# Kernel optimization log

Hardware: AMD Instinct MI355X
Metric: run time of the kernel (lower is better)

Reference implementation:

```python
import jax, jax.numpy as jnp
import numpy as np

N_HEAD = 16

def setup_inputs() -> dict:
    key = jax.random.key(0)
    ks = jax.random.split(key, 9)
    B, T, C = 4, 2048, 1024
    s = 1.0 / np.sqrt(C)
    return {
        "x":  jax.random.normal(ks[0], (B, T, C), jnp.float32),
        "Wq": jax.random.normal(ks[1], (C, C), jnp.float32) * s,
        "bq": jax.random.normal(ks[2], (C,), jnp.float32) * 0.02,
        "Wk": jax.random.normal(ks[3], (C, C), jnp.float32) * s,
        "bk": jax.random.normal(ks[4], (C,), jnp.float32) * 0.02,
        "Wv": jax.random.normal(ks[5], (C, C), jnp.float32) * s,
        "bv": jax.random.normal(ks[6], (C,), jnp.float32) * 0.02,
        "Wp": jax.random.normal(ks[7], (C, C), jnp.float32) * s,
        "bp": jax.random.normal(ks[8], (C,), jnp.float32) * 0.02,
    }

def reference(x, Wq, bq, Wk, bk, Wv, bv, Wp, bp):
    B, T, C = x.shape
    H, D = N_HEAD, C // N_HEAD
    # torch nn.Linear: y = x @ W^T + b
    q = (x @ Wq.T + bq).reshape(B, T, H, D).transpose(0, 2, 1, 3)  # [B,H,T,D]
    k = (x @ Wk.T + bk).reshape(B, T, H, D).transpose(0, 2, 1, 3)
    v = (x @ Wv.T + bv).reshape(B, T, H, D).transpose(0, 2, 1, 3)
    # full TxT causal attention (non-flash path)
    att = jnp.einsum('bhtd,bhsd->bhts', q, k) * (1.0 / np.sqrt(D))  # [B,H,T,T]
    causal = jnp.tril(jnp.ones((T, T), dtype=bool))
    att = jnp.where(causal[None, None], att, -jnp.inf)
    att = jax.nn.softmax(att, axis=-1)
    y = jnp.einsum('bhts,bhsd->bhtd', att, v)  # [B,H,T,D]
    y = y.transpose(0, 2, 1, 3).reshape(B, T, C)
    return y @ Wp.T + bp
```

## Files before the change

kernel.cpp:

```cpp
#include <hip/hip_runtime.h>

typedef __bf16 bf16_t;
typedef __bf16 bf16x8 __attribute__((ext_vector_type(8)));
typedef float f32x4 __attribute__((ext_vector_type(4)));
typedef unsigned short ushort_t;

#define T_SEQ 2048
#define C_DIM 1024
#define NH    16
#define HD    64

__device__ __forceinline__ ushort_t f2bf(float f) {
    unsigned u = __builtin_bit_cast(unsigned, f);
    u += 0x7FFFu + ((u >> 16) & 1u);
    return (ushort_t)(u >> 16);
}

__global__ __launch_bounds__(256)
void cvt_kernel(const float* __restrict__ src, ushort_t* __restrict__ dst, int n4) {
    int i = blockIdx.x * blockDim.x + threadIdx.x;
    if (i < n4) {
        float4 f = ((const float4*)src)[i];
        ushort4 u;
        u.x = f2bf(f.x); u.y = f2bf(f.y); u.z = f2bf(f.z); u.w = f2bf(f.w);
        ((ushort4*)dst)[i] = u;
    }
}

template<bool AF32, bool BF32>
__device__ __forceinline__ void gemm_core_128(const void* __restrict__ Araw,
                                              const void* __restrict__ Braw,
                                              f32x4 (&acc)[4][4]) {
    __shared__ alignas(16) ushort_t As[128 * 72];
    __shared__ alignas(16) ushort_t Ws[128 * 72];
    const int tid  = threadIdx.x;
    const int lane = tid & 63;
    const int wv   = tid >> 6;
    const int wm   = wv >> 1, wn = wv & 1;
    const int quad = lane >> 4, ln = lane & 15;
    const int m0 = blockIdx.x * 128, n0 = blockIdx.y * 128;

    f32x4 z4 = {0.f, 0.f, 0.f, 0.f};
#pragma unroll
    for (int i = 0; i < 4; i++)
#pragma unroll
        for (int j = 0; j < 4; j++) acc[i][j] = z4;

    for (int kt = 0; kt < 1024; kt += 64) {
        if (AF32) {
            const float* A = (const float*)Araw;
#pragma unroll
            for (int p = 0; p < 8; ++p) {
                int cid = p * 256 + tid;
                int row = cid >> 4, c4 = (cid & 15) * 4;
                float4 f = *(const float4*)(A + (size_t)(m0 + row) * 1024 + kt + c4);
                ushort4 u;
                u.x = f2bf(f.x); u.y = f2bf(f.y); u.z = f2bf(f.z); u.w = f2bf(f.w);
                *(ushort4*)&As[row * 72 + c4] = u;
            }
        } else {
            const bf16_t* A = (const bf16_t*)Araw;
#pragma unroll
            for (int p = 0; p < 4; ++p) {
                int cid = p * 256 + tid;
                int row = cid >> 3, c8 = (cid & 7) * 8;
                *(uint4*)&As[row * 72 + c8] =
                    *(const uint4*)(A + (size_t)(m0 + row) * 1024 + kt + c8);
            }
        }
        if (BF32) {
            const float* Bm = (const float*)Braw;
#pragma unroll
            for (int p = 0; p < 8; ++p) {
                int cid = p * 256 + tid;
                int row = cid >> 4, c4 = (cid & 15) * 4;
                float4 f = *(const float4*)(Bm + (size_t)(n0 + row) * 1024 + kt + c4);
                ushort4 u;
                u.x = f2bf(f.x); u.y = f2bf(f.y); u.z = f2bf(f.z); u.w = f2bf(f.w);
                *(ushort4*)&Ws[row * 72 + c4] = u;
            }
        } else {
            const bf16_t* Bm = (const bf16_t*)Braw;
#pragma unroll
            for (int p = 0; p < 4; ++p) {
                int cid = p * 256 + tid;
                int row = cid >> 3, c8 = (cid & 7) * 8;
                *(uint4*)&Ws[row * 72 + c8] =
                    *(const uint4*)(Bm + (size_t)(n0 + row) * 1024 + kt + c8);
            }
        }
        __syncthreads();
#pragma unroll
        for (int ks = 0; ks < 2; ++ks) {
            bf16x8 af[4], bfr[4];
#pragma unroll
            for (int i = 0; i < 4; i++)
                af[i] = *(const bf16x8*)&As[(wm * 64 + i * 16 + ln) * 72 + ks * 32 + quad * 8];
#pragma unroll
            for (int j = 0; j < 4; j++)
                bfr[j] = *(const bf16x8*)&Ws[(wn * 64 + j * 16 + ln) * 72 + ks * 32 + quad * 8];
#pragma unroll
            for (int i = 0; i < 4; i++)
#pragma unroll
                for (int j = 0; j < 4; j++)
                    acc[i][j] = __builtin_amdgcn_mfma_f32_16x16x32_bf16(af[i], bfr[j],
                                                                        acc[i][j], 0, 0, 0);
        }
        __syncthreads();
    }
}

__global__ __launch_bounds__(256, 2)
void qkv_gemm_kernel(const bf16_t* __restrict__ xb,
                     const bf16_t* __restrict__ Wqb, const float* __restrict__ bq,
                     const bf16_t* __restrict__ Wkb, const float* __restrict__ bk,
                     const bf16_t* __restrict__ Wvb, const float* __restrict__ bv,
                     ushort_t* __restrict__ Qo, ushort_t* __restrict__ Ko,
                     ushort_t* __restrict__ Vo) {
    const int z = blockIdx.z;
    const bf16_t* W   = (z == 0) ? Wqb : (z == 1) ? Wkb : Wvb;
    const float* bias = (z == 0) ? bq : (z == 1) ? bk : bv;
    ushort_t* outp    = (z == 0) ? Qo : (z == 1) ? Ko : Vo;

    f32x4 acc[4][4];
    gemm_core_128<false, false>(xb, W, acc);

    const int tid  = threadIdx.x;
    const int lane = tid & 63;
    const int wv2  = tid >> 6;
    const int wm   = wv2 >> 1, wn = wv2 & 1;
    const int quad = lane >> 4, ln = lane & 15;
    const int mbase = blockIdx.x * 128 + wm * 64;
    const int nbase = blockIdx.y * 128 + wn * 64;

#pragma unroll
    for (int j = 0; j < 4; j++) {
        int n = nbase + j * 16 + ln;
        float bj = bias[n];
        int h = n >> 6, d = n & 63;
#pragma unroll
        for (int i = 0; i < 4; i++) {
            int mr = mbase + i * 16 + quad * 4;
            int b = mr >> 11;
            int t = mr & 2047;
            if (z < 2) {
                ushort_t* op = outp + ((size_t)(b * NH + h) * T_SEQ + t) * HD + d;
#pragma unroll
                for (int r = 0; r < 4; r++)
                    op[(size_t)r * HD] = f2bf(acc[i][j][r] + bj);
            } else {
                ushort4 us;
                us.x = f2bf(acc[i][j][0] + bj);
                us.y = f2bf(acc[i][j][1] + bj);
                us.z = f2bf(acc[i][j][2] + bj);
                us.w = f2bf(acc[i][j][3] + bj);
                *(ushort4*)(outp + ((size_t)(b * NH + h) * HD + d) * T_SEQ + t) = us;
            }
        }
    }
}

__device__ __forceinline__ void attn_tile(const ushort_t* __restrict__ Ks,
                                          const ushort_t* __restrict__ Vts,
                                          ushort_t* __restrict__ PsW,
                                          bf16x8 aq0, bf16x8 aq1, bf16x8 ones,
                                          f32x4 (&o)[4], f32x4& l4,
                                          bool diag, int wv, int quad, int ln) {
    const float cscale = 0.18033688011112042f;
    f32x4 s4[4];
#pragma unroll
    for (int n16 = 0; n16 < 4; n16++) {
        f32x4 zz = {0.f, 0.f, 0.f, 0.f};
        bf16x8 bk0 = *(const bf16x8*)&Ks[(n16 * 16 + ln) * 72 + quad * 8];
        zz = __builtin_amdgcn_mfma_f32_16x16x32_bf16(aq0, bk0, zz, 0, 0, 0);
        bf16x8 bk1 = *(const bf16x8*)&Ks[(n16 * 16 + ln) * 72 + 32 + quad * 8];
        zz = __builtin_amdgcn_mfma_f32_16x16x32_bf16(aq1, bk1, zz, 0, 0, 0);
        s4[n16] = zz;
    }

#pragma unroll
    for (int n16 = 0; n16 < 4; n16++) {
#pragma unroll
        for (int r = 0; r < 4; r++) {
            float v = s4[n16][r] * cscale;
            if (diag) {
                int sg = n16 * 16 + ln;
                int qg = wv * 16 + quad * 4 + r;
                if (sg > qg) v = -1e30f;
            }
            float pv = exp2f(v);
            PsW[(quad * 4 + r) * 72 + n16 * 16 + ln] = f2bf(pv);
        }
    }

#pragma unroll
    for (int ks = 0; ks < 2; ks++) {
        bf16x8 ap = *(const bf16x8*)&PsW[ln * 72 + ks * 32 + quad * 8];
        l4 = __builtin_amdgcn_mfma_f32_16x16x32_bf16(ap, ones, l4, 0, 0, 0);
#pragma unroll
        for (int d16 = 0; d16 < 4; d16++) {
            bf16x8 bv = *(const bf16x8*)&Vts[(d16 * 16 + ln) * 72 + ks * 32 + quad * 8];
            o[d16] = __builtin_amdgcn_mfma_f32_16x16x32_bf16(ap, bv, o[d16], 0, 0, 0);
        }
    }
}

__global__ __launch_bounds__(256, 4)
void flash_kernel(const ushort_t* __restrict__ Qw, const ushort_t* __restrict__ Kw,
                  const ushort_t* __restrict__ Vt, ushort_t* __restrict__ Y) {
    __shared__ alignas(16) ushort_t Ks[64 * 72];
    __shared__ alignas(16) ushort_t Vts[64 * 72];
    __shared__ alignas(16) ushort_t Ps[4 * 16 * 72];

    const int tid  = threadIdx.x;
    const int lane = tid & 63;
    const int wv   = tid >> 6;
    const int quad = lane >> 4, ln = lane & 15;
    const int p  = blockIdx.x;
    const int bh = blockIdx.y;
    const int qa = p, qb = 31 - p;
    const int b = bh >> 4, h = bh & 15;
    ushort_t* PsW = &Ps[wv * 1152];

    bf16x8 ones;
#pragma unroll
    for (int i = 0; i < 8; i++) ones[i] = (bf16_t)1.0f;

    const ushort_t* qpa = Qw + ((size_t)bh * T_SEQ + qa * 64 + wv * 16 + ln) * HD;
    const ushort_t* qpb = Qw + ((size_t)bh * T_SEQ + qb * 64 + wv * 16 + ln) * HD;
    bf16x8 aqA0 = *(const bf16x8*)(qpa + quad * 8);
    bf16x8 aqA1 = *(const bf16x8*)(qpa + 32 + quad * 8);
    bf16x8 aqB0 = *(const bf16x8*)(qpb + quad * 8);
    bf16x8 aqB1 = *(const bf16x8*)(qpb + 32 + quad * 8);

    f32x4 oA[4], oB[4];
    f32x4 z4 = {0.f, 0.f, 0.f, 0.f};
#pragma unroll
    for (int i = 0; i < 4; i++) { oA[i] = z4; oB[i] = z4; }
    f32x4 lA4 = z4, lB4 = z4;

    const int row0 = tid >> 3, c80 = (tid & 7) * 8;
    const int row1 = (256 + tid) >> 3, c81 = c80;

    uint4 pk0, pk1, pv0, pv1;
    pk0 = *(const uint4*)(Kw + ((size_t)bh * T_SEQ + row0) * HD + c80);
    pv0 = *(const uint4*)(Vt + ((size_t)bh * HD + row0) * T_SEQ + c80);
    pk1 = *(const uint4*)(Kw + ((size_t)bh * T_SEQ + row1) * HD + c81);
    pv1 = *(const uint4*)(Vt + ((size_t)bh * HD + row1) * T_SEQ + c81);

    for (int st = 0; st <= qb; ++st) {
        __syncthreads();
        *(uint4*)&Ks[row0 * 72 + c80]  = pk0;
        *(uint4*)&Vts[row0 * 72 + c80] = pv0;
        *(uint4*)&Ks[row1 * 72 + c81]  = pk1;
        *(uint4*)&Vts[row1 * 72 + c81] = pv1;
        if (st < qb) {
            int s1 = (st + 1) * 64;
            pk0 = *(const uint4*)(Kw + ((size_t)bh * T_SEQ + s1 + row0) * HD + c80);
            pv0 = *(const uint4*)(Vt + ((size_t)bh * HD + row0) * T_SEQ + s1 + c80);
            pk1 = *(const uint4*)(Kw + ((size_t)bh * T_SEQ + s1 + row1) * HD + c81);
            pv1 = *(const uint4*)(Vt + ((size_t)bh * HD + row1) * T_SEQ + s1 + c81);
        }
        __syncthreads();

        if (st <= qa)
            attn_tile(Ks, Vts, PsW, aqA0, aqA1, ones, oA, lA4, st == qa, wv, quad, ln);
        attn_tile(Ks, Vts, PsW, aqB0, aqB1, ones, oB, lB4, st == qb, wv, quad, ln);
    }

#pragma unroll
    for (int ph = 0; ph < 2; ph++) {
        f32x4* o = ph ? oB : oA;
        f32x4 l4 = ph ? lB4 : lA4;
        int qt = ph ? qb : qa;
        f32x4 inv = {1.f / l4[0], 1.f / l4[1], 1.f / l4[2], 1.f / l4[3]};
        const int tg = qt * 64 + wv * 16 + quad * 4;
#pragma unroll
        for (int d16 = 0; d16 < 4; d16++) {
#pragma unroll
            for (int r = 0; r < 4; r++) {
                float v = o[d16][r] * inv[r];
                Y[((size_t)b * T_SEQ + tg + r) * C_DIM + h * HD + d16 * 16 + ln] = f2bf(v);
            }
        }
    }
}

__global__ __launch_bounds__(256, 2)
void proj_gemm_kernel(const bf16_t* __restrict__ Yw, const float* __restrict__ Wp,
                      const float* __restrict__ bp, float* __restrict__ out) {
    f32x4 acc[4][4];
    gemm_core_128<false, true>(Yw, Wp, acc);

    const int tid  = threadIdx.x;
    const int lane = tid & 63;
    const int wv2  = tid >> 6;
    const int wm   = wv2 >> 1, wn = wv2 & 1;
    const int quad = lane >> 4, ln = lane & 15;
    const int mbase = blockIdx.x * 128 + wm * 64;
    const int nbase = blockIdx.y * 128 + wn * 64;

#pragma unroll
    for (int j = 0; j < 4; j++) {
        int n = nbase + j * 16 + ln;
        float bj = bp[n];
#pragma unroll
        for (int i = 0; i < 4; i++) {
            int mr = mbase + i * 16 + quad * 4;
#pragma unroll
            for (int r = 0; r < 4; r++)
                out[(size_t)(mr + r) * C_DIM + n] = acc[i][j][r] + bj;
        }
    }
}

extern "C" void kernel_launch(void* const* d_in, const int* in_sizes, int n_in,
                              void* d_out, int out_size, void* d_ws, size_t ws_size,
                              hipStream_t stream) {
    const float* x  = (const float*)d_in[0];
    const float* Wq = (const float*)d_in[1];
    const float* bq = (const float*)d_in[2];
    const float* Wk = (const float*)d_in[3];
    const float* bk = (const float*)d_in[4];
    const float* Wv = (const float*)d_in[5];
    const float* bv = (const float*)d_in[6];
    const float* Wp = (const float*)d_in[7];
    const float* bp = (const float*)d_in[8];
    float* out = (float*)d_out;

    char* ws = (char*)d_ws;
    const size_t MB = (size_t)1 << 20;
    ushort_t* Qw = (ushort_t*)(ws);
    ushort_t* Kw = (ushort_t*)(ws + 16 * MB);
    ushort_t* Vt = (ushort_t*)(ws + 32 * MB);
    ushort_t* Yw = (ushort_t*)(ws + 48 * MB);

    ushort_t* xb  = (ushort_t*)out;
    ushort_t* Wqb = (ushort_t*)((char*)out + 16 * MB);
    ushort_t* Wkb = (ushort_t*)((char*)out + 18 * MB);
    ushort_t* Wvb = (ushort_t*)((char*)out + 20 * MB);

    cvt_kernel<<<8192, 256, 0, stream>>>(x,  xb,  8388608 / 4);
    cvt_kernel<<<1024, 256, 0, stream>>>(Wq, Wqb, 1048576 / 4);
    cvt_kernel<<<1024, 256, 0, stream>>>(Wk, Wkb, 1048576 / 4);
    cvt_kernel<<<1024, 256, 0, stream>>>(Wv, Wvb, 1048576 / 4);

    dim3 g1(64, 8, 3);
    qkv_gemm_kernel<<<g1, 256, 0, stream>>>((const bf16_t*)xb,
                                            (const bf16_t*)Wqb, bq,
                                            (const bf16_t*)Wkb, bk,
                                            (const bf16_t*)Wvb, bv,
                                            Qw, Kw, Vt);

    dim3 g2(16, 64);
    flash_kernel<<<g2, 256, 0, stream>>>(Qw, Kw, Vt, Yw);

    dim3 g3(64, 8, 1);
    proj_gemm_kernel<<<g3, 256, 0, stream>>>((const bf16_t*)Yw, Wp, bp, out);
}
```

Before: 291.5 us.

## Merge conversion launches, fold softmax scale into Q, store P as fp32

The four fp32-to-bf16 conversion launches become one kernel that picks its source and destination from the thread index, saving three launches. The softmax scale (log2e/sqrt(D)) is now applied to Q in the QKV GEMM epilogue, which removes a multiply per score in the attention inner loop. The per-wave P buffer in LDS changes from bf16 to fp32 with stride 68, and values are converted to bf16 when read back. This doubles the P buffer's LDS footprint and adds read-side conversions, and rounding Q after scaling shifts numerics slightly.

```diff
diff --git a/kernel.cpp b/kernel.cpp
--- a/kernel.cpp
+++ b/kernel.cpp
@@ -16,15 +16,23 @@
     return (ushort_t)(u >> 16);
 }
 
+#define X4  2097152
+#define W4  262144
 __global__ __launch_bounds__(256)
-void cvt_kernel(const float* __restrict__ src, ushort_t* __restrict__ dst, int n4) {
-    int i = blockIdx.x * blockDim.x + threadIdx.x;
-    if (i < n4) {
-        float4 f = ((const float4*)src)[i];
-        ushort4 u;
-        u.x = f2bf(f.x); u.y = f2bf(f.y); u.z = f2bf(f.z); u.w = f2bf(f.w);
-        ((ushort4*)dst)[i] = u;
-    }
+void cvt_all_kernel(const float* __restrict__ x,  const float* __restrict__ Wq,
+                    const float* __restrict__ Wk, const float* __restrict__ Wv,
+                    ushort_t* __restrict__ xb,  ushort_t* __restrict__ Wqb,
+                    ushort_t* __restrict__ Wkb, ushort_t* __restrict__ Wvb) {
+    int i = blockIdx.x * 256 + threadIdx.x;
+    const float* src; ushort_t* dst; int off;
+    if (i < X4)                { src = x;  dst = xb;  off = i; }
+    else if (i < X4 + W4)      { src = Wq; dst = Wqb; off = i - X4; }
+    else if (i < X4 + 2 * W4)  { src = Wk; dst = Wkb; off = i - X4 - W4; }
+    else                       { src = Wv; dst = Wvb; off = i - X4 - 2 * W4; }
+    float4 f = ((const float4*)src)[off];
+    ushort4 u;
+    u.x = f2bf(f.x); u.y = f2bf(f.y); u.z = f2bf(f.z); u.w = f2bf(f.w);
+    ((ushort4*)dst)[off] = u;
 }
 
 template<bool AF32, bool BF32>
@@ -121,6 +129,7 @@
     const bf16_t* W   = (z == 0) ? Wqb : (z == 1) ? Wkb : Wvb;
     const float* bias = (z == 0) ? bq : (z == 1) ? bk : bv;
     ushort_t* outp    = (z == 0) ? Qo : (z == 1) ? Ko : Vo;
+    const float fs    = (z == 0) ? 0.18033688011112042f : 1.0f;
 
     f32x4 acc[4][4];
     gemm_core_128<false, false>(xb, W, acc);
@@ -147,7 +156,7 @@
                 ushort_t* op = outp + ((size_t)(b * NH + h) * T_SEQ + t) * HD + d;
 #pragma unroll
                 for (int r = 0; r < 4; r++)
-                    op[(size_t)r * HD] = f2bf(acc[i][j][r] + bj);
+                    op[(size_t)r * HD] = f2bf((acc[i][j][r] + bj) * fs);
             } else {
                 ushort4 us;
                 us.x = f2bf(acc[i][j][0] + bj);
@@ -160,13 +169,13 @@
     }
 }
 
+#define PSTR 68
 __device__ __forceinline__ void attn_tile(const ushort_t* __restrict__ Ks,
                                           const ushort_t* __restrict__ Vts,
-                                          ushort_t* __restrict__ PsW,
+                                          float* __restrict__ PsW,
                                           bf16x8 aq0, bf16x8 aq1, bf16x8 ones,
                                           f32x4 (&o)[4], f32x4& l4,
                                           bool diag, int wv, int quad, int ln) {
-    const float cscale = 0.18033688011112042f;
     f32x4 s4[4];
 #pragma unroll
     for (int n16 = 0; n16 < 4; n16++) {
@@ -182,20 +191,23 @@
     for (int n16 = 0; n16 < 4; n16++) {
 #pragma unroll
         for (int r = 0; r < 4; r++) {
-            float v = s4[n16][r] * cscale;
+            float v = s4[n16][r];
             if (diag) {
                 int sg = n16 * 16 + ln;
                 int qg = wv * 16 + quad * 4 + r;
                 if (sg > qg) v = -1e30f;
             }
-            float pv = exp2f(v);
-            PsW[(quad * 4 + r) * 72 + n16 * 16 + ln] = f2bf(pv);
+            PsW[(quad * 4 + r) * PSTR + n16 * 16 + ln] = exp2f(v);
         }
     }
 
 #pragma unroll
     for (int ks = 0; ks < 2; ks++) {
-        bf16x8 ap = *(const bf16x8*)&PsW[ln * 72 + ks * 32 + quad * 8];
+        f32x4 p0 = *(const f32x4*)&PsW[ln * PSTR + ks * 32 + quad * 8];
+        f32x4 p1 = *(const f32x4*)&PsW[ln * PSTR + ks * 32 + quad * 8 + 4];
+        bf16x8 ap;
+#pragma unroll
+        for (int j = 0; j < 4; j++) { ap[j] = (bf16_t)p0[j]; ap[4 + j] = (bf16_t)p1[j]; }
         l4 = __builtin_amdgcn_mfma_f32_16x16x32_bf16(ap, ones, l4, 0, 0, 0);
 #pragma unroll
         for (int d16 = 0; d16 < 4; d16++) {
@@ -210,7 +222,7 @@
                   const ushort_t* __restrict__ Vt, ushort_t* __restrict__ Y) {
     __shared__ alignas(16) ushort_t Ks[64 * 72];
     __shared__ alignas(16) ushort_t Vts[64 * 72];
-    __shared__ alignas(16) ushort_t Ps[4 * 16 * 72];
+    __shared__ alignas(16) float    Ps[4 * 16 * PSTR];
 
     const int tid  = threadIdx.x;
     const int lane = tid & 63;
@@ -220,7 +232,7 @@
     const int bh = blockIdx.y;
     const int qa = p, qb = 31 - p;
     const int b = bh >> 4, h = bh & 15;
-    ushort_t* PsW = &Ps[wv * 1152];
+    float* PsW = &Ps[wv * 16 * PSTR];
 
     bf16x8 ones;
 #pragma unroll
@@ -340,10 +352,7 @@
     ushort_t* Wkb = (ushort_t*)((char*)out + 18 * MB);
     ushort_t* Wvb = (ushort_t*)((char*)out + 20 * MB);
 
-    cvt_kernel<<<8192, 256, 0, stream>>>(x,  xb,  8388608 / 4);
-    cvt_kernel<<<1024, 256, 0, stream>>>(Wq, Wqb, 1048576 / 4);
-    cvt_kernel<<<1024, 256, 0, stream>>>(Wk, Wkb, 1048576 / 4);
-    cvt_kernel<<<1024, 256, 0, stream>>>(Wv, Wvb, 1048576 / 4);
+    cvt_all_kernel<<<11264, 256, 0, stream>>>(x, Wq, Wk, Wv, xb, Wqb, Wkb, Wvb);
 
     dim3 g1(64, 8, 3);
     qkv_gemm_kernel<<<g1, 256, 0, stream>>>((const bf16_t*)xb,
```

Measured after the change: 287.9 us. Within noise of the previous version (-1.2%).
